# Optimization experiments

Measured on AMD Instinct MI355X. Metric: run time of the kernel, lower is better.

Reference implementation:

```python
import jax, jax.numpy as jnp
import numpy as np

D_MODEL = 1024
N_HEAD = 16
D_HEAD = D_MODEL // N_HEAD


def setup_inputs() -> dict:
    key = jax.random.key(0)
    ks = jax.random.split(key, 5)
    x = jax.random.normal(ks[0], (4, 2048, D_MODEL), dtype=jnp.float32)
    # qkv linear: weight [3*d_model, d_model], bias [3*d_model] (torch convention)
    w_qkv = jax.random.normal(ks[1], (3 * D_MODEL, D_MODEL), dtype=jnp.float32) / np.sqrt(D_MODEL)
    b_qkv = jnp.zeros((3 * D_MODEL,), dtype=jnp.float32)
    w_proj = jax.random.normal(ks[2], (D_MODEL, D_MODEL), dtype=jnp.float32) / np.sqrt(D_MODEL)
    b_proj = jnp.zeros((D_MODEL,), dtype=jnp.float32)
    return {"x": x, "w_qkv": w_qkv, "b_qkv": b_qkv, "w_proj": w_proj, "b_proj": b_proj}


def reference(x, w_qkv, b_qkv, w_proj, b_proj):
    B, T, C = x.shape
    qkv = x @ w_qkv.T + b_qkv  # [B,T,3C]
    q, k, v = jnp.split(qkv, 3, axis=-1)
    # [B, H, T, Dh]
    q = q.reshape(B, T, N_HEAD, D_HEAD).transpose(0, 2, 1, 3)
    k = k.reshape(B, T, N_HEAD, D_HEAD).transpose(0, 2, 1, 3)
    v = v.reshape(B, T, N_HEAD, D_HEAD).transpose(0, 2, 1, 3)
    att = jnp.einsum('bhqd,bhkd->bhqk', q, k) / jnp.sqrt(jnp.float32(D_HEAD))
    causal = jnp.tril(jnp.ones((T, T), dtype=bool))  # [T,T]
    att = jnp.where(causal, att, -jnp.inf)
    att = jax.nn.softmax(att, axis=-1)
    y = jnp.einsum('bhqk,bhkd->bhqd', att, v)  # [B,H,T,Dh]
    y = y.transpose(0, 2, 1, 3).reshape(B, T, C)
    return y @ w_proj.T + b_proj
```

## Files before the change

kernel.cpp:

```cpp
#include <hip/hip_runtime.h>
#include <hip/hip_bf16.h>

#define DEV static __device__ __forceinline__

typedef __attribute__((ext_vector_type(8))) short short8;
typedef __attribute__((ext_vector_type(4))) short short4v;
typedef __attribute__((ext_vector_type(4))) float float4v;
typedef __attribute__((ext_vector_type(4))) int int4v;

DEV unsigned short f2bf(float f) {
  unsigned int u = __builtin_bit_cast(unsigned int, f);
  u = (u + 0x7fffu + ((u >> 16) & 1u)) >> 16;
  return (unsigned short)u;
}

DEV __attribute__((address_space(3))) void* to_lds(void* p) {
  return (__attribute__((address_space(3))) void*)p;
}
DEV const __attribute__((address_space(1))) void* to_glb(const void* p) {
  return (const __attribute__((address_space(1))) void*)p;
}

DEV float4v zero4() { float4v z = {0.f, 0.f, 0.f, 0.f}; return z; }

DEV float ex2(float x) {
  float r;
  asm("v_exp_f32 %0, %1" : "=v"(r) : "v"(x));
  return r;
}
DEV unsigned int cvtpk(float lo, float hi) {
  unsigned int r;
  asm("v_cvt_pk_bf16_f32 %0, %1, %2" : "=v"(r) : "v"(lo), "v"(hi));
  return r;
}

__global__ __launch_bounds__(256)
void f32_to_bf16_kn(const float* __restrict__ src, unsigned short* __restrict__ dst, int n) {
  int i = (blockIdx.x * blockDim.x + threadIdx.x) * 4;
  int stride = gridDim.x * blockDim.x * 4;
  for (; i < n; i += stride) {
    float4v v = *reinterpret_cast<const float4v*>(src + i);
    short4v o;
    o[0] = (short)f2bf(v[0]);
    o[1] = (short)f2bf(v[1]);
    o[2] = (short)f2bf(v[2]);
    o[3] = (short)f2bf(v[3]);
    *reinterpret_cast<short4v*>(dst + i) = o;
  }
}

template<int OUT_F32>
__global__ __launch_bounds__(256, 2)
void gemm_bt_kn(const unsigned short* __restrict__ A, const unsigned short* __restrict__ B,
                const float* __restrict__ bias, void* __restrict__ Cout,
                int M, int N, int K) {
  __shared__ unsigned short sA[128 * 64];
  __shared__ unsigned short sB[128 * 64];
  const int t = threadIdx.x;
  const int wave = t >> 6, lane = t & 63;
  const int wm = wave >> 1, wn = wave & 1;
  const int m0 = blockIdx.y * 128, n0 = blockIdx.x * 128;
  const int l15 = lane & 15, l4 = lane >> 4;

  float4v acc[4][4];
#pragma unroll
  for (int i = 0; i < 4; i++)
#pragma unroll
    for (int j = 0; j < 4; j++) acc[i][j] = zero4();

  const int row_s = t >> 3;
  const int cols_s = ((t & 7) ^ ((t >> 3) & 7)) * 8;

  for (int k0 = 0; k0 < K; k0 += 64) {
    __syncthreads();
#pragma unroll
    for (int i = 0; i < 4; i++) {
      const unsigned short* ga = &A[(size_t)(m0 + row_s + i * 32) * K + k0 + cols_s];
      __builtin_amdgcn_global_load_lds(to_glb(ga), to_lds(&sA[(i * 4096 + wave * 1024) / 2]), 16, 0, 0);
    }
#pragma unroll
    for (int i = 0; i < 4; i++) {
      const unsigned short* gb = &B[(size_t)(n0 + row_s + i * 32) * K + k0 + cols_s];
      __builtin_amdgcn_global_load_lds(to_glb(gb), to_lds(&sB[(i * 4096 + wave * 1024) / 2]), 16, 0, 0);
    }
    __syncthreads();
#pragma unroll
    for (int kc = 0; kc < 2; kc++) {
      short8 af[4], bf[4];
#pragma unroll
      for (int mf = 0; mf < 4; mf++) {
        int off = ((wm * 64 + mf * 16 + l15) * 128 + kc * 64 + l4 * 16) ^ ((l15 & 7) << 4);
        af[mf] = *reinterpret_cast<const short8*>((const char*)sA + off);
      }
#pragma unroll
      for (int nf = 0; nf < 4; nf++) {
        int off = ((wn * 64 + nf * 16 + l15) * 128 + kc * 64 + l4 * 16) ^ ((l15 & 7) << 4);
        bf[nf] = *reinterpret_cast<const short8*>((const char*)sB + off);
      }
      __builtin_amdgcn_s_setprio(1);
#pragma unroll
      for (int mf = 0; mf < 4; mf++)
#pragma unroll
        for (int nf = 0; nf < 4; nf++)
          acc[mf][nf] = __builtin_amdgcn_mfma_f32_16x16x32_bf16(af[mf], bf[nf], acc[mf][nf], 0, 0, 0);
      __builtin_amdgcn_s_setprio(0);
    }
  }

#pragma unroll
  for (int mf = 0; mf < 4; mf++) {
#pragma unroll
    for (int nf = 0; nf < 4; nf++) {
#pragma unroll
      for (int r = 0; r < 4; r++) {
        int row = m0 + wm * 64 + mf * 16 + l4 * 4 + r;
        int col = n0 + wn * 64 + nf * 16 + l15;
        float v = acc[mf][nf][r] + bias[col];
        if (OUT_F32)
          ((float*)Cout)[(size_t)row * N + col] = v;
        else
          ((unsigned short*)Cout)[(size_t)row * N + col] = f2bf(v);
      }
    }
  }
}

__global__ __launch_bounds__(256, 2)
void attn_kn(const unsigned short* __restrict__ qkv, unsigned short* __restrict__ y) {
  __shared__ unsigned short sK[2][4096];
  __shared__ unsigned short sVT[2][4096];
  __shared__ unsigned short sP[4][2048];
  const int t = threadIdx.x;
  const int wave = t >> 6, lane = t & 63;
  const int l15 = lane & 15, l4 = lane >> 4;
  const int bh = blockIdx.x;
  const int pairp = blockIdx.y;
  const int b = bh >> 4, h = bh & 15;
  const int T = 2048;
  const size_t base = (size_t)b * T * 3072;
  const unsigned short* Qp = qkv + base + h * 64;
  const unsigned short* Kp = qkv + base + 1024 + h * 64;
  const unsigned short* Vp = qkv + base + 2048 + h * 64;
  const float scl = 0.125f * 1.44269504089f;

  const int vkp = t >> 3;
  const int vd0 = (t & 7) * 8;

  int4v va, vb;
  auto stage_k = [&](int kv0, int bi) {
#pragma unroll
    for (int i = 0; i < 2; i++) {
      int unit = t + i * 256;
      int row = unit >> 3, sl = unit & 7;
      const unsigned short* g = Kp + (size_t)(kv0 + row) * 3072 + (sl ^ (row & 7)) * 8;
      __builtin_amdgcn_global_load_lds(to_glb(g), to_lds(&sK[bi][unit * 8]), 16, 0, 0);
    }
  };
  auto vload = [&](int kv0) {
    const unsigned short* g = Vp + (size_t)(kv0 + vkp * 2) * 3072 + vd0;
    va = *reinterpret_cast<const int4v*>(g);
    vb = *reinterpret_cast<const int4v*>(g + 3072);
  };
  auto vstore = [&](int bi) {
    const unsigned short* pa = (const unsigned short*)&va;
    const unsigned short* pb = (const unsigned short*)&vb;
#pragma unroll
    for (int j = 0; j < 8; j++) {
      int d = vd0 + j;
      unsigned int pk = (unsigned int)pa[j] | ((unsigned int)pb[j] << 16);
      int off = (d * 128 + vkp * 4) ^ (((d ^ (d >> 3)) & 7) << 4);
      *(unsigned int*)((char*)sVT[bi] + off) = pk;
    }
  };

  for (int ph = 0; ph < 2; ph++) {
    const int qt = ph ? (15 - pairp) : pairp;
    const int q0w = qt * 128 + wave * 32;
    const int q_end = q0w + 31;

    short8 qf[2][2];
#pragma unroll
    for (int m = 0; m < 2; m++)
#pragma unroll
      for (int kc = 0; kc < 2; kc++)
        qf[m][kc] = *reinterpret_cast<const short8*>(
            &Qp[(size_t)(q0w + m * 16 + l15) * 3072 + kc * 32 + l4 * 8]);

    float4v o_acc[2][4];
#pragma unroll
    for (int m = 0; m < 2; m++)
#pragma unroll
      for (int f = 0; f < 4; f++) o_acc[m][f] = zero4();
    float m_r[2] = {-1e30f, -1e30f};
    float l_r[2] = {0.f, 0.f};

    const int nt = qt * 2 + 2;
    stage_k(0, 0);
    vload(0);
    vstore(0);
    __syncthreads();

    for (int ti = 0; ti < nt; ti++) {
      const int cur = ti & 1;
      const int kv0 = ti * 64;
      const bool last = (ti + 1 == nt);
      if (!last) { stage_k(kv0 + 64, cur ^ 1); vload(kv0 + 64); }

      if (kv0 <= q_end) {
        const char* Kb = (const char*)sK[cur];
        const char* Vb = (const char*)sVT[cur];
        char* Pb = (char*)sP[wave];

        float4v st[2][4];
#pragma unroll
        for (int m = 0; m < 2; m++)
#pragma unroll
          for (int c = 0; c < 4; c++) st[m][c] = zero4();
#pragma unroll
        for (int kc = 0; kc < 2; kc++) {
          short8 ka[4];
#pragma unroll
          for (int c = 0; c < 4; c++) {
            int off = ((c * 16 + l15) * 128 + kc * 64 + l4 * 16) ^ ((l15 & 7) << 4);
            ka[c] = *reinterpret_cast<const short8*>(Kb + off);
          }
          __builtin_amdgcn_s_setprio(1);
#pragma unroll
          for (int c = 0; c < 4; c++) {
            st[0][c] = __builtin_amdgcn_mfma_f32_16x16x32_bf16(ka[c], qf[0][kc], st[0][c], 0, 0, 0);
            st[1][c] = __builtin_amdgcn_mfma_f32_16x16x32_bf16(ka[c], qf[1][kc], st[1][c], 0, 0, 0);
          }
          __builtin_amdgcn_s_setprio(0);
        }

#pragma unroll
        for (int m = 0; m < 2; m++) {
          const int qrow = q0w + m * 16 + l15;
          const bool needmask = (kv0 + 63 > q0w + m * 16);
          if (needmask) {
#pragma unroll
            for (int c = 0; c < 4; c++)
#pragma unroll
              for (int r = 0; r < 4; r++) {
                int kv = kv0 + c * 16 + l4 * 4 + r;
                if (kv > qrow) st[m][c][r] = -1e30f;
              }
          }
          float pm = -1e30f;
#pragma unroll
          for (int c = 0; c < 4; c++)
#pragma unroll
            for (int r = 0; r < 4; r++) pm = fmaxf(pm, st[m][c][r]);
          pm = fmaxf(pm, __shfl_xor(pm, 16, 64));
          pm = fmaxf(pm, __shfl_xor(pm, 32, 64));

          float mold = m_r[m];
          float mm = mold;
          if (!__all(pm <= mold + 44.0f)) {
            mm = fmaxf(mold, pm);
            float sc = ex2((mold - mm) * scl);
            m_r[m] = mm;
            l_r[m] *= sc;
            float scr[4];
#pragma unroll
            for (int r = 0; r < 4; r++) scr[r] = __shfl(sc, l4 * 4 + r, 64);
#pragma unroll
            for (int f = 0; f < 4; f++)
#pragma unroll
              for (int r = 0; r < 4; r++) o_acc[m][f][r] *= scr[r];
          }
          const float mscl = mm * scl;
          float ps = 0.f;
#pragma unroll
          for (int c = 0; c < 4; c++)
#pragma unroll
            for (int r = 0; r < 4; r++) {
              float p = ex2(fmaf(st[m][c][r], scl, -mscl));
              st[m][c][r] = p;
              ps += p;
            }
          ps += __shfl_xor(ps, 16, 64);
          ps += __shfl_xor(ps, 32, 64);
          l_r[m] += ps;

#pragma unroll
          for (int c = 0; c < 4; c++) {
            unsigned long long w =
                (unsigned long long)cvtpk(st[m][c][0], st[m][c][1]) |
                ((unsigned long long)cvtpk(st[m][c][2], st[m][c][3]) << 32);
            int off = ((m * 16 + l15) * 128 + (c * 16 + l4 * 4) * 2) ^ ((l15 & 7) << 4);
            *(unsigned long long*)(Pb + off) = w;
          }
        }
        asm volatile("s_waitcnt lgkmcnt(0)" ::: "memory");
        __builtin_amdgcn_sched_barrier(0);

#pragma unroll
        for (int kc = 0; kc < 2; kc++) {
          short8 pa[2];
#pragma unroll
          for (int m = 0; m < 2; m++) {
            int off = ((m * 16 + l15) * 128 + kc * 64 + l4 * 16) ^ ((l15 & 7) << 4);
            pa[m] = *reinterpret_cast<const short8*>(Pb + off);
          }
#pragma unroll
          for (int f = 0; f < 4; f++) {
            int d = f * 16 + l15;
            int off = (d * 128 + kc * 64 + l4 * 16) ^ (((d ^ (d >> 3)) & 7) << 4);
            short8 vbf = *reinterpret_cast<const short8*>(Vb + off);
            __builtin_amdgcn_s_setprio(1);
            o_acc[0][f] = __builtin_amdgcn_mfma_f32_16x16x32_bf16(pa[0], vbf, o_acc[0][f], 0, 0, 0);
            o_acc[1][f] = __builtin_amdgcn_mfma_f32_16x16x32_bf16(pa[1], vbf, o_acc[1][f], 0, 0, 0);
            __builtin_amdgcn_s_setprio(0);
          }
        }
      }
      if (!last) vstore(cur ^ 1);
      __syncthreads();
    }

    unsigned short* yb = y + (size_t)b * T * 1024 + h * 64;
#pragma unroll
    for (int m = 0; m < 2; m++) {
      float lr[4];
#pragma unroll
      for (int r = 0; r < 4; r++) lr[r] = 1.0f / __shfl(l_r[m], l4 * 4 + r, 64);
#pragma unroll
      for (int f = 0; f < 4; f++)
#pragma unroll
        for (int r = 0; r < 4; r++) {
          int q = q0w + m * 16 + l4 * 4 + r;
          yb[(size_t)q * 1024 + f * 16 + l15] = f2bf(o_acc[m][f][r] * lr[r]);
        }
    }
  }
}

extern "C" void kernel_launch(void* const* d_in, const int* in_sizes, int n_in,
                              void* d_out, int out_size, void* d_ws, size_t ws_size,
                              hipStream_t stream) {
  const float* x = (const float*)d_in[0];
  const float* w_qkv = (const float*)d_in[1];
  const float* b_qkv = (const float*)d_in[2];
  const float* w_proj = (const float*)d_in[3];
  const float* b_proj = (const float*)d_in[4];
  float* out = (float*)d_out;
  char* ws = (char*)d_ws;

  const int M = 4 * 2048;
  unsigned short* x_bf = (unsigned short*)ws;
  unsigned short* wqkv_bf = (unsigned short*)(ws + (22ull << 20));
  unsigned short* wproj_bf = (unsigned short*)(ws + (28ull << 20));
  unsigned short* qkv = (unsigned short*)(ws + (30ull << 20));
  unsigned short* y_bf = x_bf;

  f32_to_bf16_kn<<<2048, 256, 0, stream>>>(x, x_bf, M * 1024);
  f32_to_bf16_kn<<<1024, 256, 0, stream>>>(w_qkv, wqkv_bf, 3072 * 1024);
  f32_to_bf16_kn<<<512, 256, 0, stream>>>(w_proj, wproj_bf, 1024 * 1024);

  gemm_bt_kn<0><<<dim3(3072 / 128, M / 128), 256, 0, stream>>>(x_bf, wqkv_bf, b_qkv, qkv, M, 3072, 1024);

  attn_kn<<<dim3(64, 8), 256, 0, stream>>>(qkv, y_bf);

  gemm_bt_kn<1><<<dim3(1024 / 128, M / 128), 256, 0, stream>>>(y_bf, wproj_bf, b_proj, out, M, 1024, 1024);
}
```

Measured before the change: 180.8 us.

## Fold softmax scale into QKV GEMM, shrink attention q-tile, MFMA row sums

The softmax scale times log2(e) is folded into the Q columns in the QKV GEMM epilogue, which removes the per-element scale FMA from the attention loop. The attention kernel now uses 64-row query tiles with 16 rows per wave instead of 128/32. The grid doubles to 64x16 and launch bounds go to 4 blocks per CU, with a smaller P scratch buffer. Row sums of P are computed with an extra MFMA against a ones vector instead of shuffles, and the lazy-rescale threshold is adjusted to the log2 domain. Smaller tiles give more parallelism and occupancy, at the cost of more K/V reloads and more barriers per unit of work.

```diff
diff --git a/kernel.cpp b/kernel.cpp
--- a/kernel.cpp
+++ b/kernel.cpp
@@ -49,7 +49,7 @@
   }
 }
 
-template<int OUT_F32>
+template<int OUT_F32, int SCALE_Q>
 __global__ __launch_bounds__(256, 2)
 void gemm_bt_kn(const unsigned short* __restrict__ A, const unsigned short* __restrict__ B,
                 const float* __restrict__ bias, void* __restrict__ Cout,
@@ -116,6 +116,7 @@
         int row = m0 + wm * 64 + mf * 16 + l4 * 4 + r;
         int col = n0 + wn * 64 + nf * 16 + l15;
         float v = acc[mf][nf][r] + bias[col];
+        if (SCALE_Q && col < 1024) v *= 0.18033688f;
         if (OUT_F32)
           ((float*)Cout)[(size_t)row * N + col] = v;
         else
@@ -125,11 +126,11 @@
   }
 }
 
-__global__ __launch_bounds__(256, 2)
+__global__ __launch_bounds__(256, 4)
 void attn_kn(const unsigned short* __restrict__ qkv, unsigned short* __restrict__ y) {
   __shared__ unsigned short sK[2][4096];
   __shared__ unsigned short sVT[2][4096];
-  __shared__ unsigned short sP[4][2048];
+  __shared__ unsigned short sP[4][1024];
   const int t = threadIdx.x;
   const int wave = t >> 6, lane = t & 63;
   const int l15 = lane & 15, l4 = lane >> 4;
@@ -141,7 +142,10 @@
   const unsigned short* Qp = qkv + base + h * 64;
   const unsigned short* Kp = qkv + base + 1024 + h * 64;
   const unsigned short* Vp = qkv + base + 2048 + h * 64;
-  const float scl = 0.125f * 1.44269504089f;
+
+  short8 ones;
+#pragma unroll
+  for (int j = 0; j < 8; j++) ones[j] = (short)0x3F80;
 
   const int vkp = t >> 3;
   const int vd0 = (t & 7) * 8;
@@ -174,27 +178,23 @@
   };
 
   for (int ph = 0; ph < 2; ph++) {
-    const int qt = ph ? (15 - pairp) : pairp;
-    const int q0w = qt * 128 + wave * 32;
-    const int q_end = q0w + 31;
-
-    short8 qf[2][2];
-#pragma unroll
-    for (int m = 0; m < 2; m++)
-#pragma unroll
-      for (int kc = 0; kc < 2; kc++)
-        qf[m][kc] = *reinterpret_cast<const short8*>(
-            &Qp[(size_t)(q0w + m * 16 + l15) * 3072 + kc * 32 + l4 * 8]);
-
-    float4v o_acc[2][4];
-#pragma unroll
-    for (int m = 0; m < 2; m++)
-#pragma unroll
-      for (int f = 0; f < 4; f++) o_acc[m][f] = zero4();
-    float m_r[2] = {-1e30f, -1e30f};
-    float l_r[2] = {0.f, 0.f};
-
-    const int nt = qt * 2 + 2;
+    const int qt = ph ? (31 - pairp) : pairp;
+    const int q0w = qt * 64 + wave * 16;
+    const int qrow = q0w + l15;
+
+    short8 qf[2];
+#pragma unroll
+    for (int kc = 0; kc < 2; kc++)
+      qf[kc] = *reinterpret_cast<const short8*>(
+          &Qp[(size_t)(q0w + l15) * 3072 + kc * 32 + l4 * 8]);
+
+    float4v o_acc[4];
+#pragma unroll
+    for (int f = 0; f < 4; f++) o_acc[f] = zero4();
+    float4v acc_l = zero4();
+    float m_r = -1e30f;
+
+    const int nt = qt + 1;
     stage_k(0, 0);
     vload(0);
     vstore(0);
@@ -206,133 +206,111 @@
       const bool last = (ti + 1 == nt);
       if (!last) { stage_k(kv0 + 64, cur ^ 1); vload(kv0 + 64); }
 
-      if (kv0 <= q_end) {
-        const char* Kb = (const char*)sK[cur];
-        const char* Vb = (const char*)sVT[cur];
-        char* Pb = (char*)sP[wave];
-
-        float4v st[2][4];
-#pragma unroll
-        for (int m = 0; m < 2; m++)
-#pragma unroll
-          for (int c = 0; c < 4; c++) st[m][c] = zero4();
-#pragma unroll
-        for (int kc = 0; kc < 2; kc++) {
-          short8 ka[4];
-#pragma unroll
-          for (int c = 0; c < 4; c++) {
-            int off = ((c * 16 + l15) * 128 + kc * 64 + l4 * 16) ^ ((l15 & 7) << 4);
-            ka[c] = *reinterpret_cast<const short8*>(Kb + off);
+      const char* Kb = (const char*)sK[cur];
+      const char* Vb = (const char*)sVT[cur];
+      char* Pb = (char*)sP[wave];
+
+      float4v st[4];
+#pragma unroll
+      for (int c = 0; c < 4; c++) st[c] = zero4();
+#pragma unroll
+      for (int kc = 0; kc < 2; kc++) {
+        short8 ka[4];
+#pragma unroll
+        for (int c = 0; c < 4; c++) {
+          int off = ((c * 16 + l15) * 128 + kc * 64 + l4 * 16) ^ ((l15 & 7) << 4);
+          ka[c] = *reinterpret_cast<const short8*>(Kb + off);
+        }
+        __builtin_amdgcn_s_setprio(1);
+#pragma unroll
+        for (int c = 0; c < 4; c++)
+          st[c] = __builtin_amdgcn_mfma_f32_16x16x32_bf16(ka[c], qf[kc], st[c], 0, 0, 0);
+        __builtin_amdgcn_s_setprio(0);
+      }
+
+      if (kv0 + 63 > q0w) {
+#pragma unroll
+        for (int c = 0; c < 4; c++)
+#pragma unroll
+          for (int r = 0; r < 4; r++) {
+            int kv = kv0 + c * 16 + l4 * 4 + r;
+            if (kv > qrow) st[c][r] = -1e30f;
           }
-          __builtin_amdgcn_s_setprio(1);
-#pragma unroll
-          for (int c = 0; c < 4; c++) {
-            st[0][c] = __builtin_amdgcn_mfma_f32_16x16x32_bf16(ka[c], qf[0][kc], st[0][c], 0, 0, 0);
-            st[1][c] = __builtin_amdgcn_mfma_f32_16x16x32_bf16(ka[c], qf[1][kc], st[1][c], 0, 0, 0);
-          }
-          __builtin_amdgcn_s_setprio(0);
+      }
+      float pm = -1e30f;
+#pragma unroll
+      for (int c = 0; c < 4; c++)
+#pragma unroll
+        for (int r = 0; r < 4; r++) pm = fmaxf(pm, st[c][r]);
+      pm = fmaxf(pm, __shfl_xor(pm, 16, 64));
+      pm = fmaxf(pm, __shfl_xor(pm, 32, 64));
+
+      float mold = m_r;
+      float mm = mold;
+      if (!__all(pm <= mold + 11.5409f)) {
+        mm = fmaxf(mold, pm);
+        float sc = ex2(mold - mm);
+        m_r = mm;
+        float scr[4];
+#pragma unroll
+        for (int r = 0; r < 4; r++) scr[r] = __shfl(sc, l4 * 4 + r, 64);
+#pragma unroll
+        for (int r = 0; r < 4; r++) {
+          acc_l[r] *= scr[r];
+#pragma unroll
+          for (int f = 0; f < 4; f++) o_acc[f][r] *= scr[r];
         }
-
-#pragma unroll
-        for (int m = 0; m < 2; m++) {
-          const int qrow = q0w + m * 16 + l15;
-          const bool needmask = (kv0 + 63 > q0w + m * 16);
-          if (needmask) {
-#pragma unroll
-            for (int c = 0; c < 4; c++)
-#pragma unroll
-              for (int r = 0; r < 4; r++) {
-                int kv = kv0 + c * 16 + l4 * 4 + r;
-                if (kv > qrow) st[m][c][r] = -1e30f;
-              }
-          }
-          float pm = -1e30f;
-#pragma unroll
-          for (int c = 0; c < 4; c++)
-#pragma unroll
-            for (int r = 0; r < 4; r++) pm = fmaxf(pm, st[m][c][r]);
-          pm = fmaxf(pm, __shfl_xor(pm, 16, 64));
-          pm = fmaxf(pm, __shfl_xor(pm, 32, 64));
-
-          float mold = m_r[m];
-          float mm = mold;
-          if (!__all(pm <= mold + 44.0f)) {
-            mm = fmaxf(mold, pm);
-            float sc = ex2((mold - mm) * scl);
-            m_r[m] = mm;
-            l_r[m] *= sc;
-            float scr[4];
-#pragma unroll
-            for (int r = 0; r < 4; r++) scr[r] = __shfl(sc, l4 * 4 + r, 64);
-#pragma unroll
-            for (int f = 0; f < 4; f++)
-#pragma unroll
-              for (int r = 0; r < 4; r++) o_acc[m][f][r] *= scr[r];
-          }
-          const float mscl = mm * scl;
-          float ps = 0.f;
-#pragma unroll
-          for (int c = 0; c < 4; c++)
-#pragma unroll
-            for (int r = 0; r < 4; r++) {
-              float p = ex2(fmaf(st[m][c][r], scl, -mscl));
-              st[m][c][r] = p;
-              ps += p;
-            }
-          ps += __shfl_xor(ps, 16, 64);
-          ps += __shfl_xor(ps, 32, 64);
-          l_r[m] += ps;
-
-#pragma unroll
-          for (int c = 0; c < 4; c++) {
-            unsigned long long w =
-                (unsigned long long)cvtpk(st[m][c][0], st[m][c][1]) |
-                ((unsigned long long)cvtpk(st[m][c][2], st[m][c][3]) << 32);
-            int off = ((m * 16 + l15) * 128 + (c * 16 + l4 * 4) * 2) ^ ((l15 & 7) << 4);
-            *(unsigned long long*)(Pb + off) = w;
-          }
+      }
+#pragma unroll
+      for (int c = 0; c < 4; c++)
+#pragma unroll
+        for (int r = 0; r < 4; r++) st[c][r] = ex2(st[c][r] - mm);
+
+#pragma unroll
+      for (int c = 0; c < 4; c++) {
+        unsigned long long w =
+            (unsigned long long)cvtpk(st[c][0], st[c][1]) |
+            ((unsigned long long)cvtpk(st[c][2], st[c][3]) << 32);
+        int off = (l15 * 128 + (c * 16 + l4 * 4) * 2) ^ ((l15 & 7) << 4);
+        *(unsigned long long*)(Pb + off) = w;
+      }
+      asm volatile("s_waitcnt lgkmcnt(0)" ::: "memory");
+      __builtin_amdgcn_sched_barrier(0);
+
+#pragma unroll
+      for (int kc = 0; kc < 2; kc++) {
+        int poff = (l15 * 128 + kc * 64 + l4 * 16) ^ ((l15 & 7) << 4);
+        short8 pa = *reinterpret_cast<const short8*>(Pb + poff);
+        short8 vbf[4];
+#pragma unroll
+        for (int f = 0; f < 4; f++) {
+          int d = f * 16 + l15;
+          int off = (d * 128 + kc * 64 + l4 * 16) ^ (((d ^ (d >> 3)) & 7) << 4);
+          vbf[f] = *reinterpret_cast<const short8*>(Vb + off);
         }
-        asm volatile("s_waitcnt lgkmcnt(0)" ::: "memory");
-        __builtin_amdgcn_sched_barrier(0);
-
-#pragma unroll
-        for (int kc = 0; kc < 2; kc++) {
-          short8 pa[2];
-#pragma unroll
-          for (int m = 0; m < 2; m++) {
-            int off = ((m * 16 + l15) * 128 + kc * 64 + l4 * 16) ^ ((l15 & 7) << 4);
-            pa[m] = *reinterpret_cast<const short8*>(Pb + off);
-          }
-#pragma unroll
-          for (int f = 0; f < 4; f++) {
-            int d = f * 16 + l15;
-            int off = (d * 128 + kc * 64 + l4 * 16) ^ (((d ^ (d >> 3)) & 7) << 4);
-            short8 vbf = *reinterpret_cast<const short8*>(Vb + off);
-            __builtin_amdgcn_s_setprio(1);
-            o_acc[0][f] = __builtin_amdgcn_mfma_f32_16x16x32_bf16(pa[0], vbf, o_acc[0][f], 0, 0, 0);
-            o_acc[1][f] = __builtin_amdgcn_mfma_f32_16x16x32_bf16(pa[1], vbf, o_acc[1][f], 0, 0, 0);
-            __builtin_amdgcn_s_setprio(0);
-          }
-        }
-      }
+        __builtin_amdgcn_s_setprio(1);
+#pragma unroll
+        for (int f = 0; f < 4; f++)
+          o_acc[f] = __builtin_amdgcn_mfma_f32_16x16x32_bf16(pa, vbf[f], o_acc[f], 0, 0, 0);
+        acc_l = __builtin_amdgcn_mfma_f32_16x16x32_bf16(pa, ones, acc_l, 0, 0, 0);
+        __builtin_amdgcn_s_setprio(0);
+      }
+
       if (!last) vstore(cur ^ 1);
       __syncthreads();
     }
 
     unsigned short* yb = y + (size_t)b * T * 1024 + h * 64;
-#pragma unroll
-    for (int m = 0; m < 2; m++) {
-      float lr[4];
-#pragma unroll
-      for (int r = 0; r < 4; r++) lr[r] = 1.0f / __shfl(l_r[m], l4 * 4 + r, 64);
-#pragma unroll
-      for (int f = 0; f < 4; f++)
-#pragma unroll
-        for (int r = 0; r < 4; r++) {
-          int q = q0w + m * 16 + l4 * 4 + r;
-          yb[(size_t)q * 1024 + f * 16 + l15] = f2bf(o_acc[m][f][r] * lr[r]);
-        }
-    }
+    float lr[4];
+#pragma unroll
+    for (int r = 0; r < 4; r++) lr[r] = 1.0f / acc_l[r];
+#pragma unroll
+    for (int f = 0; f < 4; f++)
+#pragma unroll
+      for (int r = 0; r < 4; r++) {
+        int q = q0w + l4 * 4 + r;
+        yb[(size_t)q * 1024 + f * 16 + l15] = f2bf(o_acc[f][r] * lr[r]);
+      }
   }
 }
 
@@ -358,9 +336,9 @@
   f32_to_bf16_kn<<<1024, 256, 0, stream>>>(w_qkv, wqkv_bf, 3072 * 1024);
   f32_to_bf16_kn<<<512, 256, 0, stream>>>(w_proj, wproj_bf, 1024 * 1024);
 
-  gemm_bt_kn<0><<<dim3(3072 / 128, M / 128), 256, 0, stream>>>(x_bf, wqkv_bf, b_qkv, qkv, M, 3072, 1024);
-
-  attn_kn<<<dim3(64, 8), 256, 0, stream>>>(qkv, y_bf);
-
-  gemm_bt_kn<1><<<dim3(1024 / 128, M / 128), 256, 0, stream>>>(y_bf, wproj_bf, b_proj, out, M, 1024, 1024);
-}
+  gemm_bt_kn<0, 1><<<dim3(3072 / 128, M / 128), 256, 0, stream>>>(x_bf, wqkv_bf, b_qkv, qkv, M, 3072, 1024);
+
+  attn_kn<<<dim3(64, 16), 256, 0, stream>>>(qkv, y_bf);
+
+  gemm_bt_kn<1, 0><<<dim3(1024 / 128, M / 128), 256, 0, stream>>>(y_bf, wproj_bf, b_proj, out, M, 1024, 1024);
+}
```

Result: faster. 173.0 us (-4.3%).
